# Kernel optimization log

Measured on AMD Instinct MI355X. Metric: run time of the kernel, lower is better.

Reference implementation:

```python
import jax, jax.numpy as jnp
import numpy as np

DIM = 768
NUM_HEADS = 12
HEAD_DIM = DIM // NUM_HEADS
SCALE = HEAD_DIM ** (-0.5)


def setup_inputs() -> dict:
    key = jax.random.key(0)
    ks = jax.random.split(key, 8)
    B, Nq, Nk, Nv = 2, 2048, 2048, 2048
    init = 0.02
    return {
        "xq": jax.random.normal(ks[0], (B, Nq, DIM), dtype=jnp.float32),
        "xk": jax.random.normal(ks[1], (B, Nk, DIM), dtype=jnp.float32),
        "xv": jax.random.normal(ks[2], (B, Nv, DIM), dtype=jnp.float32),
        # torch nn.Linear weights are [out_features, in_features]; qkv_bias=False
        "Wq": jax.random.normal(ks[3], (DIM, DIM), dtype=jnp.float32) * init,
        "Wk": jax.random.normal(ks[4], (DIM, DIM), dtype=jnp.float32) * init,
        "Wv": jax.random.normal(ks[5], (DIM, DIM), dtype=jnp.float32) * init,
        "Wp": jax.random.normal(ks[6], (DIM, DIM), dtype=jnp.float32) * init,
        "bp": jax.random.normal(ks[7], (DIM,), dtype=jnp.float32) * init,
    }


def reference(xq, xk, xv, Wq, Wk, Wv, Wp, bp):
    B, Nq, C = xq.shape
    H, D = NUM_HEADS, HEAD_DIM
    # linear projections (torch Linear: x @ W.T), split heads -> [B, H, N, D]
    q = (xq @ Wq.T).reshape(B, Nq, H, D).transpose(0, 2, 1, 3)
    k = (xk @ Wk.T).reshape(B, xk.shape[1], H, D).transpose(0, 2, 1, 3)
    v = (xv @ Wv.T).reshape(B, xv.shape[1], H, D).transpose(0, 2, 1, 3)
    # attention scores [B, H, Nq, Nk]
    attn = jnp.einsum("bhqd,bhkd->bhqk", q, k) * SCALE
    attn = jax.nn.softmax(attn, axis=-1)
    # weighted values -> merge heads [B, Nq, C]
    out = jnp.einsum("bhqk,bhkd->bhqd", attn, v)
    out = out.transpose(0, 2, 1, 3).reshape(B, Nq, C)
    return out @ Wp.T + bp
```

## Files before the change

kernel.cpp:

```cpp
#include <hip/hip_runtime.h>
#include <hip/hip_bf16.h>


#define NSEQ 2048
#define CDIM 768
#define NH   12
#define HD   64
#define MTOT 4096
#define XEL  (MTOT*CDIM)
#define WEL  (CDIM*CDIM)
#define X8   (XEL/8)
#define W8   (WEL/8)
#define QSCALE 0.18033688011112042f

typedef __attribute__((ext_vector_type(8))) short bf16x8;
typedef __attribute__((ext_vector_type(4))) float floatx4;
typedef __attribute__((ext_vector_type(16))) float floatx16;
typedef __attribute__((ext_vector_type(4))) unsigned int uintx4;

static __device__ __forceinline__ unsigned short f2bf(float f) {
  union { float f; unsigned int u; } v; v.f = f;
  return (unsigned short)((v.u + 0x8000u) >> 16);
}
static __device__ __forceinline__ unsigned pk2bf(float a, float b) {
  unsigned ua = __float_as_uint(a) + 0x8000u;
  unsigned ub = __float_as_uint(b) + 0x8000u;
  return __builtin_amdgcn_perm(ub, ua, 0x07060302);
}

static __device__ __forceinline__ void lds16(const void* g, void* l) {
  __builtin_amdgcn_global_load_lds(
      (const __attribute__((address_space(1))) unsigned int*)g,
      (__attribute__((address_space(3))) unsigned int*)l, 16, 0, 0);
}

#define LGKM0_SB()  do { asm volatile("s_waitcnt lgkmcnt(0)" ::: "memory"); \
                         __builtin_amdgcn_sched_barrier(0); } while (0)
#define VMCNT0()    asm volatile("s_waitcnt vmcnt(0)" ::: "memory")
#define BARRIER()   __builtin_amdgcn_s_barrier()
#define SB0()       __builtin_amdgcn_sched_barrier(0)

__global__ __launch_bounds__(256) void cast_all(
    const float* __restrict__ xq, const float* __restrict__ xk,
    const float* __restrict__ xv, const float* __restrict__ wq,
    const float* __restrict__ wk, const float* __restrict__ wv,
    const float* __restrict__ wp,
    unsigned short* __restrict__ Xq, unsigned short* __restrict__ Xk,
    unsigned short* __restrict__ Xv, unsigned short* __restrict__ Wq,
    unsigned short* __restrict__ Wk, unsigned short* __restrict__ Wv,
    unsigned short* __restrict__ Wp) {
  int i = blockIdx.x * 256 + threadIdx.x;
  const float* s; unsigned short* d; int off;
  if (i < 3 * X8) {
    int t = i / X8; off = i - t * X8;
    s = (t == 0) ? xq : (t == 1) ? xk : xv;
    d = (t == 0) ? Xq : (t == 1) ? Xk : Xv;
  } else {
    int j = i - 3 * X8; int t = j / W8; off = j - t * W8;
    s = (t == 0) ? wq : (t == 1) ? wk : (t == 2) ? wv : wp;
    d = (t == 0) ? Wq : (t == 1) ? Wk : (t == 2) ? Wv : Wp;
  }
  const float4* sp = (const float4*)s + (size_t)off * 2;
  float4 a = sp[0], b = sp[1];
  uint4 o;
  o.x = pk2bf(a.x, a.y); o.y = pk2bf(a.z, a.w);
  o.z = pk2bf(b.x, b.y); o.w = pk2bf(b.z, b.w);
  *(uint4*)(d + (size_t)off * 8) = o;
}

__global__ __launch_bounds__(256) void gemm_qkv(
    const unsigned short* __restrict__ Xq, const unsigned short* __restrict__ Xk,
    const unsigned short* __restrict__ Xv, const unsigned short* __restrict__ Wq,
    const unsigned short* __restrict__ Wk, const unsigned short* __restrict__ Wv,
    unsigned short* __restrict__ Qo, unsigned short* __restrict__ Ko,
    unsigned short* __restrict__ Vo) {
  int i0 = blockIdx.x;
  int mg = i0 & 7; int t0 = i0 >> 3;
  int z = t0 % 3; int u = t0 / 3;
  int xn = u & 7, ysub = u >> 3;
  int y = mg * 4 + ysub;
  const unsigned short* A; const unsigned short* B; int am0, bn0, RA;
  if (z == 0)      { A = Xq; B = Wq; am0 = y * 128; bn0 = xn * 96; RA = 128; }
  else if (z == 1) { A = Xk; B = Wk; am0 = y * 128; bn0 = xn * 96; RA = 128; }
  else             { A = Wv; B = Xv; am0 = xn * 96; bn0 = y * 128; RA = 96; }
  __shared__ __align__(16) unsigned short S[224 * 64];
  int tid = threadIdx.x, lane = tid & 63, wave = tid >> 6;
  int quad = lane >> 4, l15 = lane & 15, l7 = l15 & 7;

  const unsigned short* gptr[7]; int ldo[7];
#pragma unroll
  for (int i = 0; i < 7; i++) {
    int idx = i * 256 + tid;
    int row = idx >> 3, c = (idx & 7) ^ (row & 7);
    gptr[i] = (row < RA ? A + (size_t)(am0 + row) * CDIM
                        : B + (size_t)(bn0 + row - RA) * CDIM) + c * 8;
    ldo[i] = idx * 8;
  }
  floatx4 acc[12];
#pragma unroll
  for (int i = 0; i < 12; i++) acc[i] = (floatx4){0.f, 0.f, 0.f, 0.f};

#pragma unroll
  for (int i = 0; i < 7; i++) lds16(gptr[i], &S[ldo[i]]);
  VMCNT0();
  BARRIER();

  if (z < 2) {
    int wm = (wave >> 1) * 64, wn = (wave & 1) * 48;
    for (int k0 = 0; k0 < CDIM; k0 += 64) {
      bf16x8 af[2][4], bfr[2][3];
#pragma unroll
      for (int ks = 0; ks < 2; ks++) {
        int csw = ((ks * 4 + quad) ^ l7) * 8;
#pragma unroll
        for (int i = 0; i < 4; i++)
          af[ks][i] = *(const bf16x8*)&S[(wm + i * 16 + l15) * 64 + csw];
#pragma unroll
        for (int j = 0; j < 3; j++)
          bfr[ks][j] = *(const bf16x8*)&S[(128 + wn + j * 16 + l15) * 64 + csw];
      }
      LGKM0_SB();
      BARRIER();
      if (k0 + 64 < CDIM) {
#pragma unroll
        for (int i = 0; i < 7; i++) lds16(gptr[i] + k0 + 64, &S[ldo[i]]);
      }
      SB0();
#pragma unroll
      for (int ks = 0; ks < 2; ks++)
#pragma unroll
        for (int mi = 0; mi < 4; mi++)
#pragma unroll
          for (int ni = 0; ni < 3; ni++)
            acc[mi * 3 + ni] = __builtin_amdgcn_mfma_f32_16x16x32_bf16(
                af[ks][mi], bfr[ks][ni], acc[mi * 3 + ni], 0, 0, 0);
      VMCNT0();
      BARRIER();
    }
#pragma unroll
    for (int mi = 0; mi < 4; mi++)
#pragma unroll
      for (int ni = 0; ni < 3; ni++)
#pragma unroll
        for (int r = 0; r < 4; r++) {
          int grow = am0 + wm + mi * 16 + quad * 4 + r;
          int gcol = bn0 + wn + ni * 16 + l15;
          float v = acc[mi * 3 + ni][r];
          int b = grow >> 11, nq = grow & 2047, h = gcol >> 6, dd = gcol & 63;
          if (z == 0)
            Qo[((size_t)(b * NH + h) * NSEQ + nq) * HD + dd] = f2bf(v * QSCALE);
          else
            Ko[((size_t)(b * NH + h) * NSEQ + nq) * HD + dd] = f2bf(v);
        }
  } else {
    int wm = (wave & 1) * 48, wn = (wave >> 1) * 64;
    for (int k0 = 0; k0 < CDIM; k0 += 64) {
      bf16x8 af[2][3], bfr[2][4];
#pragma unroll
      for (int ks = 0; ks < 2; ks++) {
        int csw = ((ks * 4 + quad) ^ l7) * 8;
#pragma unroll
        for (int i = 0; i < 3; i++)
          af[ks][i] = *(const bf16x8*)&S[(wm + i * 16 + l15) * 64 + csw];
#pragma unroll
        for (int j = 0; j < 4; j++)
          bfr[ks][j] = *(const bf16x8*)&S[(96 + wn + j * 16 + l15) * 64 + csw];
      }
      LGKM0_SB();
      BARRIER();
      if (k0 + 64 < CDIM) {
#pragma unroll
        for (int i = 0; i < 7; i++) lds16(gptr[i] + k0 + 64, &S[ldo[i]]);
      }
      SB0();
#pragma unroll
      for (int ks = 0; ks < 2; ks++)
#pragma unroll
        for (int mi = 0; mi < 3; mi++)
#pragma unroll
          for (int ni = 0; ni < 4; ni++)
            acc[mi * 4 + ni] = __builtin_amdgcn_mfma_f32_16x16x32_bf16(
                af[ks][mi], bfr[ks][ni], acc[mi * 4 + ni], 0, 0, 0);
      VMCNT0();
      BARRIER();
    }
#pragma unroll
    for (int mi = 0; mi < 3; mi++)
#pragma unroll
      for (int ni = 0; ni < 4; ni++)
#pragma unroll
        for (int r = 0; r < 4; r++) {
          int o = am0 + wm + mi * 16 + quad * 4 + r;
          int mgl = bn0 + wn + ni * 16 + l15;
          int b = mgl >> 11, nq = mgl & 2047;
          Vo[((size_t)b * CDIM + o) * NSEQ + nq] = f2bf(acc[mi * 4 + ni][r]);
        }
  }
}

__global__ __launch_bounds__(256, 3) void attn_kernel(
    const unsigned short* __restrict__ Q, const unsigned short* __restrict__ K,
    const unsigned short* __restrict__ Vt, unsigned short* __restrict__ ctx) {
  int i0 = blockIdx.x;
  int xcd = i0 & 7; int t0 = i0 >> 3;
  int bh = xcd * 3 + (t0 >> 5);
  int qt = t0 & 31;
  int tid = threadIdx.x, lane = tid & 63, wave = tid >> 6;
  int half = wave >> 1, qsub = wave & 1;
  int l31 = lane & 31, hi = lane >> 5;
  __shared__ __align__(16) unsigned short Ks[2][64 * 64];
  __shared__ __align__(16) unsigned short Vs[2][64 * 64];
  __shared__ float Lbuf[64];

  const unsigned short* Qg = Q + ((size_t)bh * NSEQ + qt * 64 + qsub * 32) * HD;
  const unsigned short* Kg = K + ((size_t)bh * NSEQ + half * 1024) * HD;
  const unsigned short* Vg = Vt + (size_t)bh * HD * NSEQ + half * 1024;

  bf16x8 qf[4];
#pragma unroll
  for (int dc = 0; dc < 4; dc++)
    qf[dc] = *(const bf16x8*)(Qg + l31 * HD + dc * 16 + hi * 8);

  int tid2 = tid & 127;
  int kgo[4], vgo[4], ldst[4];
#pragma unroll
  for (int i = 0; i < 4; i++) {
    int idx = i * 128 + tid2;
    int R = idx >> 3, c = (idx & 7) ^ (R & 7);
    kgo[i] = R * HD + c * 8;
    vgo[i] = R * NSEQ + c * 8;
    ldst[i] = idx * 8;
  }
  unsigned short* Ksh = Ks[half];
  unsigned short* Vsh = Vs[half];

  floatx16 o[2];
#pragma unroll
  for (int dt = 0; dt < 2; dt++) o[dt] = (floatx16)(0.f);
  float l_acc = 0.f;

#pragma unroll
  for (int i = 0; i < 4; i++) {
    lds16(Kg + kgo[i], &Ksh[ldst[i]]);
    lds16(Vg + vgo[i], &Vsh[ldst[i]]);
  }
  VMCNT0();
  BARRIER();

  for (int t = 0; t < 16; t++) {
    bf16x8 kf[2][4];
#pragma unroll
    for (int kb = 0; kb < 2; kb++)
#pragma unroll
      for (int dc = 0; dc < 4; dc++) {
        int R = kb * 32 + l31, c = dc * 2 + hi;
        kf[kb][dc] = *(const bf16x8*)&Ksh[R * 64 + ((c ^ (R & 7)) * 8)];
      }
    bf16x8 vf[2][4];
#pragma unroll
    for (int dt = 0; dt < 2; dt++)
#pragma unroll
      for (int j = 0; j < 4; j++) {
        int R = dt * 32 + l31, c = j * 2 + hi;
        vf[dt][j] = *(const bf16x8*)&Vsh[R * 64 + ((c ^ (R & 7)) * 8)];
      }
    LGKM0_SB();
    BARRIER();
    if (t < 15) {
      int k0n = (t + 1) * 64;
#pragma unroll
      for (int i = 0; i < 4; i++) {
        lds16(Kg + (size_t)k0n * HD + kgo[i], &Ksh[ldst[i]]);
        lds16(Vg + k0n + vgo[i], &Vsh[ldst[i]]);
      }
    }
    SB0();
#pragma unroll
    for (int kb = 0; kb < 2; kb++) {
      floatx16 st = (floatx16)(0.f);
#pragma unroll
      for (int dc = 0; dc < 4; dc++)
        st = __builtin_amdgcn_mfma_f32_32x32x16_bf16(kf[kb][dc], qf[dc], st, 0, 0, 0);
      float p[16];
#pragma unroll
      for (int r = 0; r < 16; r++) p[r] = __builtin_exp2f(st[r]);
      l_acc += ((p[0] + p[1]) + (p[2] + p[3])) + ((p[4] + p[5]) + (p[6] + p[7])) +
               (((p[8] + p[9]) + (p[10] + p[11])) + ((p[12] + p[13]) + (p[14] + p[15])));
      unsigned w[8];
#pragma unroll
      for (int i = 0; i < 8; i++) w[i] = pk2bf(p[2 * i], p[2 * i + 1]);
#pragma unroll
      for (int kvs = 0; kvs < 2; kvs++) {
        unsigned a0 = w[kvs * 4 + 0], b0 = w[kvs * 4 + 2];
        unsigned a1 = w[kvs * 4 + 1], b1 = w[kvs * 4 + 3];
        asm volatile("v_permlane32_swap_b32 %0, %1" : "+v"(a0), "+v"(b0));
        asm volatile("v_permlane32_swap_b32 %0, %1" : "+v"(a1), "+v"(b1));
        uintx4 pw; pw[0] = a0; pw[1] = a1; pw[2] = b0; pw[3] = b1;
        bf16x8 pb = *(bf16x8*)&pw;
#pragma unroll
        for (int dt = 0; dt < 2; dt++)
          o[dt] = __builtin_amdgcn_mfma_f32_32x32x16_bf16(
              vf[dt][kb * 2 + kvs], pb, o[dt], 0, 0, 0);
      }
    }
    VMCNT0();
    BARRIER();
  }

  unsigned lu = __float_as_uint(l_acc), lv = __float_as_uint(l_acc);
  asm volatile("v_permlane32_swap_b32 %0, %1" : "+v"(lu), "+v"(lv));
  float lfull = __uint_as_float(lu) + __uint_as_float(lv);

  float* Obuf = (float*)&Ks[0][0];
  int q = qsub * 32 + l31;
  if (half == 1) {
#pragma unroll
    for (int dt = 0; dt < 2; dt++)
#pragma unroll
      for (int rq = 0; rq < 4; rq++) {
        int ch = (dt * 8 + rq * 2 + hi) ^ (l31 & 15);
        floatx4 v4 = {o[dt][rq * 4 + 0], o[dt][rq * 4 + 1],
                      o[dt][rq * 4 + 2], o[dt][rq * 4 + 3]};
        *(floatx4*)&Obuf[q * 64 + ch * 4] = v4;
      }
    if (lane < 32) Lbuf[qsub * 32 + lane] = lfull;
  }
  __syncthreads();
  if (half == 0) {
    int b = bh / NH, h = bh - b * NH;
    float inv = 1.f / (lfull + Lbuf[q]);
    int qrow = qt * 64 + q;
#pragma unroll
    for (int dt = 0; dt < 2; dt++)
#pragma unroll
      for (int rq = 0; rq < 4; rq++) {
        int ch = (dt * 8 + rq * 2 + hi) ^ (l31 & 15);
        floatx4 ob = *(floatx4*)&Obuf[q * 64 + ch * 4];
        float v0 = (o[dt][rq * 4 + 0] + ob[0]) * inv;
        float v1 = (o[dt][rq * 4 + 1] + ob[1]) * inv;
        float v2 = (o[dt][rq * 4 + 2] + ob[2]) * inv;
        float v3 = (o[dt][rq * 4 + 3] + ob[3]) * inv;
        size_t gbase = (size_t)(b * NSEQ + qrow) * CDIM + h * HD +
                       dt * 32 + rq * 8 + hi * 4;
        *(uint2*)&ctx[gbase] = make_uint2(pk2bf(v0, v1), pk2bf(v2, v3));
      }
  }
}

__global__ __launch_bounds__(256) void gemm_out(
    const unsigned short* __restrict__ A, const unsigned short* __restrict__ B,
    const float* __restrict__ bias, float* __restrict__ out) {
  int i0 = blockIdx.x;
  int mg = i0 & 7; int t0 = i0 >> 3;
  int n0 = (t0 & 7) * 96;
  int m0 = (mg * 8 + (t0 >> 3)) * 64;
  __shared__ __align__(16) unsigned short S[160 * 128];
  int tid = threadIdx.x, lane = tid & 63, wave = tid >> 6;
  int quad = lane >> 4, l15 = lane & 15, l7 = l15 & 7;
  int wm = (wave >> 1) * 32, wn = (wave & 1) * 48;
  floatx4 acc[6];
#pragma unroll
  for (int i = 0; i < 6; i++) acc[i] = (floatx4){0.f, 0.f, 0.f, 0.f};

  int sro[10]; const unsigned short* sgp[10];
#pragma unroll
  for (int i = 0; i < 10; i++) {
    int idx = i * 256 + tid;
    int R = idx >> 4, c4 = idx & 15;
    int cs = (c4 & 8) | ((c4 & 7) ^ (R & 7));
    sgp[i] = ((R < 64) ? A + (size_t)(m0 + R) * CDIM
                       : B + (size_t)(n0 + R - 64) * CDIM) + cs * 8;
    sro[i] = idx * 8;
  }
#pragma unroll
  for (int i = 0; i < 10; i++) lds16(sgp[i], &S[sro[i]]);
  VMCNT0();
  BARRIER();

  for (int k0 = 0; k0 < CDIM; k0 += 128) {
    bf16x8 af[4][2], bfr[4][3];
#pragma unroll
    for (int ks = 0; ks < 4; ks++) {
      int c = ks * 4 + quad;
      int csw = ((c & 8) | ((c & 7) ^ l7)) * 8;
#pragma unroll
      for (int i = 0; i < 2; i++)
        af[ks][i] = *(const bf16x8*)&S[(wm + i * 16 + l15) * 128 + csw];
#pragma unroll
      for (int j = 0; j < 3; j++)
        bfr[ks][j] = *(const bf16x8*)&S[(64 + wn + j * 16 + l15) * 128 + csw];
    }
    LGKM0_SB();
    BARRIER();
    if (k0 + 128 < CDIM) {
#pragma unroll
      for (int i = 0; i < 10; i++) lds16(sgp[i] + k0 + 128, &S[sro[i]]);
    }
    SB0();
#pragma unroll
    for (int ks = 0; ks < 4; ks++)
#pragma unroll
      for (int mi = 0; mi < 2; mi++)
#pragma unroll
        for (int ni = 0; ni < 3; ni++)
          acc[mi * 3 + ni] = __builtin_amdgcn_mfma_f32_16x16x32_bf16(
              af[ks][mi], bfr[ks][ni], acc[mi * 3 + ni], 0, 0, 0);
    VMCNT0();
    BARRIER();
  }
  float bv[3];
#pragma unroll
  for (int ni = 0; ni < 3; ni++) bv[ni] = bias[n0 + wn + ni * 16 + l15];
#pragma unroll
  for (int mi = 0; mi < 2; mi++)
#pragma unroll
    for (int ni = 0; ni < 3; ni++)
#pragma unroll
      for (int r = 0; r < 4; r++) {
        int grow = m0 + wm + mi * 16 + quad * 4 + r;
        int gcol = n0 + wn + ni * 16 + l15;
        out[(size_t)grow * CDIM + gcol] = acc[mi * 3 + ni][r] + bv[ni];
      }
}

extern "C" void kernel_launch(void* const* d_in, const int* in_sizes, int n_in,
                              void* d_out, int out_size, void* d_ws, size_t ws_size,
                              hipStream_t stream) {
  const float* xq = (const float*)d_in[0];
  const float* xk = (const float*)d_in[1];
  const float* xv = (const float*)d_in[2];
  const float* wq = (const float*)d_in[3];
  const float* wk = (const float*)d_in[4];
  const float* wv = (const float*)d_in[5];
  const float* wp = (const float*)d_in[6];
  const float* bp = (const float*)d_in[7];
  float* out = (float*)d_out;

  char* p = (char*)d_ws;
  unsigned short* Xq = (unsigned short*)p; p += (size_t)XEL * 2;
  unsigned short* Xk = (unsigned short*)p; p += (size_t)XEL * 2;
  unsigned short* Xv = (unsigned short*)p; p += (size_t)XEL * 2;
  unsigned short* Wq = (unsigned short*)p; p += (size_t)WEL * 2;
  unsigned short* Wk = (unsigned short*)p; p += (size_t)WEL * 2;
  unsigned short* Wv = (unsigned short*)p; p += (size_t)WEL * 2;
  unsigned short* Wp = (unsigned short*)p; p += (size_t)WEL * 2;
  unsigned short* Qb = (unsigned short*)p; p += (size_t)XEL * 2;
  unsigned short* Kb = (unsigned short*)p; p += (size_t)XEL * 2;
  unsigned short* Vb = (unsigned short*)p; p += (size_t)XEL * 2;
  unsigned short* Cx = (unsigned short*)p; p += (size_t)XEL * 2;

  cast_all<<<(3 * X8 + 4 * W8) / 256, 256, 0, stream>>>(
      xq, xk, xv, wq, wk, wv, wp, Xq, Xk, Xv, Wq, Wk, Wv, Wp);

  gemm_qkv<<<768, 256, 0, stream>>>(
      Xq, Xk, Xv, Wq, Wk, Wv, Qb, Kb, Vb);

  attn_kernel<<<768, 256, 0, stream>>>(Qb, Kb, Vb, Cx);

  gemm_out<<<512, 256, 0, stream>>>(Cx, Wp, bp, out);
}
```

Measured before the change: 173.5 us.

## Split attention KV range four ways per wave, removing per-iteration block barriers

Each of the four waves now owns all 64 queries and a private quarter of the key/value sequence, staging its own 32-key K/V tiles in LDS. Because no tile is shared between waves, the per-iteration block barriers become wave-local waits. The partial outputs and row sums are then combined in a three-step LDS tree reduction. This doubles the output accumulators per wave, so launch bounds drop from 3 to 2 blocks per CU, and the final merge adds more synchronisation.

```diff
diff --git a/kernel.cpp b/kernel.cpp
--- a/kernel.cpp
+++ b/kernel.cpp
@@ -198,7 +198,7 @@
   }
 }
 
-__global__ __launch_bounds__(256, 3) void attn_kernel(
+__global__ __launch_bounds__(256, 2) void attn_kernel(
     const unsigned short* __restrict__ Q, const unsigned short* __restrict__ K,
     const unsigned short* __restrict__ Vt, unsigned short* __restrict__ ctx) {
   int i0 = blockIdx.x;
@@ -206,86 +206,84 @@
   int bh = xcd * 3 + (t0 >> 5);
   int qt = t0 & 31;
   int tid = threadIdx.x, lane = tid & 63, wave = tid >> 6;
-  int half = wave >> 1, qsub = wave & 1;
   int l31 = lane & 31, hi = lane >> 5;
-  __shared__ __align__(16) unsigned short Ks[2][64 * 64];
-  __shared__ __align__(16) unsigned short Vs[2][64 * 64];
-  __shared__ float Lbuf[64];
-
-  const unsigned short* Qg = Q + ((size_t)bh * NSEQ + qt * 64 + qsub * 32) * HD;
-  const unsigned short* Kg = K + ((size_t)bh * NSEQ + half * 1024) * HD;
-  const unsigned short* Vg = Vt + (size_t)bh * HD * NSEQ + half * 1024;
-
-  bf16x8 qf[4];
-#pragma unroll
-  for (int dc = 0; dc < 4; dc++)
-    qf[dc] = *(const bf16x8*)(Qg + l31 * HD + dc * 16 + hi * 8);
-
-  int tid2 = tid & 127;
-  int kgo[4], vgo[4], ldst[4];
+  __shared__ __align__(16) unsigned short SM[16384];
+  __shared__ float Lb[3][2][32];
+
+  const unsigned short* Qg = Q + ((size_t)bh * NSEQ + qt * 64) * HD;
+  const unsigned short* Kg = K + ((size_t)bh * NSEQ + wave * 512) * HD;
+  const unsigned short* Vg = Vt + (size_t)bh * HD * NSEQ + wave * 512;
+  unsigned short* Ksh = &SM[wave * 2048];
+  unsigned short* Vsh = &SM[8192 + wave * 2048];
+
+  bf16x8 qf[2][4];
+#pragma unroll
+  for (int qi = 0; qi < 2; qi++)
+#pragma unroll
+    for (int dc = 0; dc < 4; dc++)
+      qf[qi][dc] = *(const bf16x8*)(Qg + (qi * 32 + l31) * HD + dc * 16 + hi * 8);
+
+  int kgo[4], kst[4], vgo[4], vst[4];
 #pragma unroll
   for (int i = 0; i < 4; i++) {
-    int idx = i * 128 + tid2;
-    int R = idx >> 3, c = (idx & 7) ^ (R & 7);
-    kgo[i] = R * HD + c * 8;
-    vgo[i] = R * NSEQ + c * 8;
-    ldst[i] = idx * 8;
-  }
-  unsigned short* Ksh = Ks[half];
-  unsigned short* Vsh = Vs[half];
-
-  floatx16 o[2];
-#pragma unroll
-  for (int dt = 0; dt < 2; dt++) o[dt] = (floatx16)(0.f);
-  float l_acc = 0.f;
+    int idx = i * 64 + lane;
+    int Rk = idx >> 3, ck = (idx & 7) ^ (Rk & 7);
+    kgo[i] = Rk * HD + ck * 8; kst[i] = idx * 8;
+    int Rv = idx >> 2, cv = (idx & 3) ^ (Rv & 3);
+    vgo[i] = Rv * NSEQ + cv * 8; vst[i] = idx * 8;
+  }
+
+  floatx16 o[2][2];
+#pragma unroll
+  for (int qi = 0; qi < 2; qi++)
+#pragma unroll
+    for (int dt = 0; dt < 2; dt++) o[qi][dt] = (floatx16)(0.f);
+  float l_acc[2] = {0.f, 0.f};
 
 #pragma unroll
   for (int i = 0; i < 4; i++) {
-    lds16(Kg + kgo[i], &Ksh[ldst[i]]);
-    lds16(Vg + vgo[i], &Vsh[ldst[i]]);
+    lds16(Kg + kgo[i], &Ksh[kst[i]]);
+    lds16(Vg + vgo[i], &Vsh[vst[i]]);
   }
   VMCNT0();
-  BARRIER();
+  SB0();
 
   for (int t = 0; t < 16; t++) {
-    bf16x8 kf[2][4];
-#pragma unroll
-    for (int kb = 0; kb < 2; kb++)
-#pragma unroll
-      for (int dc = 0; dc < 4; dc++) {
-        int R = kb * 32 + l31, c = dc * 2 + hi;
-        kf[kb][dc] = *(const bf16x8*)&Ksh[R * 64 + ((c ^ (R & 7)) * 8)];
-      }
-    bf16x8 vf[2][4];
+    bf16x8 kf[4];
+#pragma unroll
+    for (int dc = 0; dc < 4; dc++) {
+      int c = dc * 2 + hi;
+      kf[dc] = *(const bf16x8*)&Ksh[l31 * 64 + ((c ^ (l31 & 7)) * 8)];
+    }
+    bf16x8 vf[2][2];
 #pragma unroll
     for (int dt = 0; dt < 2; dt++)
 #pragma unroll
-      for (int j = 0; j < 4; j++) {
-        int R = dt * 32 + l31, c = j * 2 + hi;
-        vf[dt][j] = *(const bf16x8*)&Vsh[R * 64 + ((c ^ (R & 7)) * 8)];
+      for (int kvs = 0; kvs < 2; kvs++) {
+        int R = dt * 32 + l31, c = kvs * 2 + hi;
+        vf[dt][kvs] = *(const bf16x8*)&Vsh[R * 32 + ((c ^ (R & 3)) * 8)];
       }
     LGKM0_SB();
-    BARRIER();
     if (t < 15) {
-      int k0n = (t + 1) * 64;
+      int off = (t + 1) * 32;
 #pragma unroll
       for (int i = 0; i < 4; i++) {
-        lds16(Kg + (size_t)k0n * HD + kgo[i], &Ksh[ldst[i]]);
-        lds16(Vg + k0n + vgo[i], &Vsh[ldst[i]]);
+        lds16(Kg + (size_t)off * HD + kgo[i], &Ksh[kst[i]]);
+        lds16(Vg + off + vgo[i], &Vsh[vst[i]]);
       }
     }
     SB0();
 #pragma unroll
-    for (int kb = 0; kb < 2; kb++) {
+    for (int qi = 0; qi < 2; qi++) {
       floatx16 st = (floatx16)(0.f);
 #pragma unroll
       for (int dc = 0; dc < 4; dc++)
-        st = __builtin_amdgcn_mfma_f32_32x32x16_bf16(kf[kb][dc], qf[dc], st, 0, 0, 0);
+        st = __builtin_amdgcn_mfma_f32_32x32x16_bf16(kf[dc], qf[qi][dc], st, 0, 0, 0);
       float p[16];
 #pragma unroll
       for (int r = 0; r < 16; r++) p[r] = __builtin_exp2f(st[r]);
-      l_acc += ((p[0] + p[1]) + (p[2] + p[3])) + ((p[4] + p[5]) + (p[6] + p[7])) +
-               (((p[8] + p[9]) + (p[10] + p[11])) + ((p[12] + p[13]) + (p[14] + p[15])));
+      l_acc[qi] += ((p[0] + p[1]) + (p[2] + p[3])) + ((p[4] + p[5]) + (p[6] + p[7])) +
+                   (((p[8] + p[9]) + (p[10] + p[11])) + ((p[12] + p[13]) + (p[14] + p[15])));
       unsigned w[8];
 #pragma unroll
       for (int i = 0; i < 8; i++) w[i] = pk2bf(p[2 * i], p[2 * i + 1]);
@@ -299,51 +297,99 @@
         bf16x8 pb = *(bf16x8*)&pw;
 #pragma unroll
         for (int dt = 0; dt < 2; dt++)
-          o[dt] = __builtin_amdgcn_mfma_f32_32x32x16_bf16(
-              vf[dt][kb * 2 + kvs], pb, o[dt], 0, 0, 0);
+          o[qi][dt] = __builtin_amdgcn_mfma_f32_32x32x16_bf16(
+              vf[dt][kvs], pb, o[qi][dt], 0, 0, 0);
       }
     }
     VMCNT0();
-    BARRIER();
-  }
-
-  unsigned lu = __float_as_uint(l_acc), lv = __float_as_uint(l_acc);
-  asm volatile("v_permlane32_swap_b32 %0, %1" : "+v"(lu), "+v"(lv));
-  float lfull = __uint_as_float(lu) + __uint_as_float(lv);
-
-  float* Obuf = (float*)&Ks[0][0];
-  int q = qsub * 32 + l31;
-  if (half == 1) {
-#pragma unroll
-    for (int dt = 0; dt < 2; dt++)
-#pragma unroll
-      for (int rq = 0; rq < 4; rq++) {
-        int ch = (dt * 8 + rq * 2 + hi) ^ (l31 & 15);
-        floatx4 v4 = {o[dt][rq * 4 + 0], o[dt][rq * 4 + 1],
-                      o[dt][rq * 4 + 2], o[dt][rq * 4 + 3]};
-        *(floatx4*)&Obuf[q * 64 + ch * 4] = v4;
-      }
-    if (lane < 32) Lbuf[qsub * 32 + lane] = lfull;
-  }
+    SB0();
+  }
+
+  float lf[2];
+#pragma unroll
+  for (int qi = 0; qi < 2; qi++) {
+    unsigned lu = __float_as_uint(l_acc[qi]), lv = __float_as_uint(l_acc[qi]);
+    asm volatile("v_permlane32_swap_b32 %0, %1" : "+v"(lu), "+v"(lv));
+    lf[qi] = __uint_as_float(lu) + __uint_as_float(lv);
+  }
+
   __syncthreads();
-  if (half == 0) {
+
+  float* Ob = (float*)&SM[0];
+  if (wave >= 2) {
+    int sl = (wave - 2) * 4096;
+#pragma unroll
+    for (int qi = 0; qi < 2; qi++) {
+      int q = qi * 32 + l31;
+#pragma unroll
+      for (int dt = 0; dt < 2; dt++)
+#pragma unroll
+        for (int rq = 0; rq < 4; rq++) {
+          int ch = (dt * 8 + rq * 2 + hi) ^ (l31 & 15);
+          floatx4 v4 = {o[qi][dt][rq * 4 + 0], o[qi][dt][rq * 4 + 1],
+                        o[qi][dt][rq * 4 + 2], o[qi][dt][rq * 4 + 3]};
+          *(floatx4*)&Ob[sl + q * 64 + ch * 4] = v4;
+        }
+      if (hi == 0) Lb[wave - 1][qi][l31] = lf[qi];
+    }
+  }
+  __syncthreads();
+  if (wave < 2) {
+#pragma unroll
+    for (int qi = 0; qi < 2; qi++) {
+      int q = qi * 32 + l31;
+#pragma unroll
+      for (int dt = 0; dt < 2; dt++)
+#pragma unroll
+        for (int rq = 0; rq < 4; rq++) {
+          int ch = (dt * 8 + rq * 2 + hi) ^ (l31 & 15);
+          floatx4 ob = *(floatx4*)&Ob[wave * 4096 + q * 64 + ch * 4];
+#pragma unroll
+          for (int j = 0; j < 4; j++) o[qi][dt][rq * 4 + j] += ob[j];
+        }
+      lf[qi] += Lb[wave + 1][qi][l31];
+    }
+  }
+  __syncthreads();
+  if (wave == 1) {
+#pragma unroll
+    for (int qi = 0; qi < 2; qi++) {
+      int q = qi * 32 + l31;
+#pragma unroll
+      for (int dt = 0; dt < 2; dt++)
+#pragma unroll
+        for (int rq = 0; rq < 4; rq++) {
+          int ch = (dt * 8 + rq * 2 + hi) ^ (l31 & 15);
+          floatx4 v4 = {o[qi][dt][rq * 4 + 0], o[qi][dt][rq * 4 + 1],
+                        o[qi][dt][rq * 4 + 2], o[qi][dt][rq * 4 + 3]};
+          *(floatx4*)&Ob[q * 64 + ch * 4] = v4;
+        }
+      if (hi == 0) Lb[0][qi][l31] = lf[qi];
+    }
+  }
+  __syncthreads();
+  if (wave == 0) {
     int b = bh / NH, h = bh - b * NH;
-    float inv = 1.f / (lfull + Lbuf[q]);
-    int qrow = qt * 64 + q;
-#pragma unroll
-    for (int dt = 0; dt < 2; dt++)
-#pragma unroll
-      for (int rq = 0; rq < 4; rq++) {
-        int ch = (dt * 8 + rq * 2 + hi) ^ (l31 & 15);
-        floatx4 ob = *(floatx4*)&Obuf[q * 64 + ch * 4];
-        float v0 = (o[dt][rq * 4 + 0] + ob[0]) * inv;
-        float v1 = (o[dt][rq * 4 + 1] + ob[1]) * inv;
-        float v2 = (o[dt][rq * 4 + 2] + ob[2]) * inv;
-        float v3 = (o[dt][rq * 4 + 3] + ob[3]) * inv;
-        size_t gbase = (size_t)(b * NSEQ + qrow) * CDIM + h * HD +
-                       dt * 32 + rq * 8 + hi * 4;
-        *(uint2*)&ctx[gbase] = make_uint2(pk2bf(v0, v1), pk2bf(v2, v3));
-      }
+#pragma unroll
+    for (int qi = 0; qi < 2; qi++) {
+      int q = qi * 32 + l31;
+      float inv = 1.f / (lf[qi] + Lb[0][qi][l31]);
+      int qrow = qt * 64 + q;
+#pragma unroll
+      for (int dt = 0; dt < 2; dt++)
+#pragma unroll
+        for (int rq = 0; rq < 4; rq++) {
+          int ch = (dt * 8 + rq * 2 + hi) ^ (l31 & 15);
+          floatx4 ob = *(floatx4*)&Ob[q * 64 + ch * 4];
+          float v0 = (o[qi][dt][rq * 4 + 0] + ob[0]) * inv;
+          float v1 = (o[qi][dt][rq * 4 + 1] + ob[1]) * inv;
+          float v2 = (o[qi][dt][rq * 4 + 2] + ob[2]) * inv;
+          float v3 = (o[qi][dt][rq * 4 + 3] + ob[3]) * inv;
+          size_t gbase = (size_t)(b * NSEQ + qrow) * CDIM + h * HD +
+                         dt * 32 + rq * 8 + hi * 4;
+          *(uint2*)&ctx[gbase] = make_uint2(pk2bf(v0, v1), pk2bf(v2, v3));
+        }
+    }
   }
 }
 
```

Measured after the change: 177.7 us. 2.4% more time.
